# Optimization experiments

Hardware: AMD Instinct MI355X
Metric: run time of the kernel (lower is better)

The kernel has to match this reference:

```python
import jax, jax.numpy as jnp
import numpy as np

HARD_ANGLE = 15.0  # degrees, from PMLoss __init__ default
NUM_CLASSES = 22
NUM_POINTS = 2048
BATCH = 32


def quat_to_rotmat(q):
    # q: [..., 4] in (w, x, y, z) order (PoseCNN convention); assumes unit norm
    w, x, y, z = q[..., 0], q[..., 1], q[..., 2], q[..., 3]
    R = jnp.stack([
        1 - 2 * (y * y + z * z), 2 * (x * y - z * w), 2 * (x * z + y * w),
        2 * (x * y + z * w), 1 - 2 * (x * x + z * z), 2 * (y * z - x * w),
        2 * (x * z - y * w), 2 * (y * z + x * w), 1 - 2 * (x * x + y * y)],
        axis=-1)
    return R.reshape(q.shape[:-1] + (3, 3))


def smooth_l1(x):
    ax = jnp.abs(x)
    return jnp.where(ax < 1.0, 0.5 * x * x, ax - 0.5)


def setup_inputs() -> dict:
    key = jax.random.key(0)
    k1, k2, k3, k4 = jax.random.split(key, 4)
    B, C, P = BATCH, NUM_CLASSES, NUM_POINTS
    # unit quaternions per (sample, class)
    q_pred = jax.random.normal(k1, (B, C, 4), dtype=jnp.float32)
    q_pred = q_pred / jnp.linalg.norm(q_pred, axis=-1, keepdims=True)
    q_gt = jax.random.normal(k2, (B, C, 4), dtype=jnp.float32)
    q_gt = q_gt / jnp.linalg.norm(q_gt, axis=-1, keepdims=True)
    prediction = q_pred.reshape(B, 4 * C)
    target = q_gt.reshape(B, 4 * C)
    # one active class per sample: weight block of ones at that class
    cls = jax.random.randint(k3, (B,), 1, C)  # skip background class 0
    weight = jnp.zeros((B, C, 4), dtype=jnp.float32)
    weight = weight.at[jnp.arange(B), cls, :].set(1.0).reshape(B, 4 * C)
    # model point clouds, roughly object-scale (~10 cm)
    points = 0.1 * jax.random.normal(k4, (C, P, 3), dtype=jnp.float32)
    # half the classes symmetric
    symmetry = (jnp.arange(C) % 2).astype(jnp.float32)
    return {"prediction": prediction, "target": target, "weight": weight,
            "points": points, "symmetry": symmetry}


def reference(prediction, target, weight, points, symmetry):
    B = prediction.shape[0]
    C = symmetry.shape[0]
    P = points.shape[1]
    # class per sample = first class with weight > 0 (CUDA scans stride-4 w slot)
    wsel = weight.reshape(B, C, 4)[:, :, 0]           # [B, C]
    cls = jnp.argmax(wsel > 0, axis=1)                # [B]
    valid = (jnp.max(wsel, axis=1) > 0)               # [B] samples with a class
    bidx = jnp.arange(B)
    q_pred = prediction.reshape(B, C, 4)[bidx, cls]   # [B, 4]
    q_gt = target.reshape(B, C, 4)[bidx, cls]         # [B, 4]
    R_pred = quat_to_rotmat(q_pred)                   # [B, 3, 3]
    R_gt = quat_to_rotmat(q_gt)
    pts = points[cls]                                 # [B, P, 3]
    p_pred = jnp.einsum('bij,bpj->bpi', R_pred, pts)  # [B, P, 3]
    p_gt = jnp.einsum('bij,bpj->bpi', R_gt, pts)      # [B, P, 3]
    # angular distance between quaternions, in degrees
    dot = jnp.abs(jnp.sum(q_pred * q_gt, axis=1))
    ang = 2.0 * jnp.arccos(jnp.clip(dot, 0.0, 1.0)) * (180.0 / jnp.pi)
    use_closest = (symmetry[cls] > 0) & (ang > HARD_ANGLE)  # [B]
    # pairwise squared distances without materializing [B,P,P,3]
    d2 = (jnp.sum(p_pred * p_pred, axis=-1)[:, :, None]
          + jnp.sum(p_gt * p_gt, axis=-1)[:, None, :]
          - 2.0 * jnp.einsum('bpi,bqi->bpq', p_pred, p_gt))  # [B, P, P]
    nn_idx = jnp.argmin(d2, axis=-1)                         # [B, P]
    p_gt_nn = jnp.take_along_axis(p_gt, nn_idx[..., None], axis=1)
    matched = jnp.where(use_closest[:, None, None], p_gt_nn, p_gt)
    diff = p_pred - matched                                   # [B, P, 3]
    per_sample = jnp.sum(smooth_l1(diff), axis=(1, 2)) * valid.astype(diff.dtype)
    loss = jnp.sum(per_sample) / jnp.asarray(B * P, dtype=diff.dtype)
    return loss
```

## Files before the change

### kernel.cpp

```cpp
#include <hip/hip_runtime.h>

#define NPTS 2048
#define QC 32
#define G  (NPTS / QC)
#define RP 8
#define HARD_COS 0.9914448613738104f
#define META_FLOATS 24
#define PRED_OFF 1024

__global__ void pm_prep(const float* __restrict__ pred,
                        const float* __restrict__ tgt,
                        const float* __restrict__ wgt,
                        const float* __restrict__ sym,
                        float* __restrict__ ws,
                        float* __restrict__ out,
                        int B, int C) {
    int b = blockIdx.x * blockDim.x + threadIdx.x;
    if (b == 0) out[0] = 0.0f;
    if (b >= B) return;

    int cls = 0; float valid = 0.0f;
    for (int c = 0; c < C; ++c) {
        if (wgt[b * 4 * C + c * 4] > 0.0f) { cls = c; valid = 1.0f; break; }
    }
    const float* qp = pred + b * 4 * C + cls * 4;
    const float* qg = tgt  + b * 4 * C + cls * 4;
    float pw = qp[0], px = qp[1], py = qp[2], pz = qp[3];
    float gw = qg[0], gx = qg[1], gy = qg[2], gz = qg[3];

    float* o = ws + (size_t)b * META_FLOATS;
    o[0] = 1.f - 2.f * (py * py + pz * pz);
    o[1] = 2.f * (px * py - pz * pw);
    o[2] = 2.f * (px * pz + py * pw);
    o[3] = 2.f * (px * py + pz * pw);
    o[4] = 1.f - 2.f * (px * px + pz * pz);
    o[5] = 2.f * (py * pz - px * pw);
    o[6] = 2.f * (px * pz - py * pw);
    o[7] = 2.f * (py * pz + px * pw);
    o[8] = 1.f - 2.f * (px * px + py * py);
    o[9]  = 1.f - 2.f * (gy * gy + gz * gz);
    o[10] = 2.f * (gx * gy - gz * gw);
    o[11] = 2.f * (gx * gz + gy * gw);
    o[12] = 2.f * (gx * gy + gz * gw);
    o[13] = 1.f - 2.f * (gx * gx + gz * gz);
    o[14] = 2.f * (gy * gz - gx * gw);
    o[15] = 2.f * (gx * gz - gy * gw);
    o[16] = 2.f * (gy * gz + gx * gw);
    o[17] = 1.f - 2.f * (gx * gx + gy * gy);

    float dot = fabsf(pw * gw + px * gx + py * gy + pz * gz);
    dot = fminf(fmaxf(dot, 0.0f), 1.0f);
    float uc = (sym[cls] > 0.0f && dot < HARD_COS) ? 1.0f : 0.0f;
    o[18] = (float)cls;
    o[19] = valid;
    o[20] = uc;
}

__global__ __launch_bounds__(256) void pm_rotate(const float* __restrict__ points,
                                                 float* __restrict__ ws,
                                                 int gt_off) {
    const int b = blockIdx.y;
    const int side = blockIdx.x;
    const float* o = ws + (size_t)b * META_FLOATS;
    if (o[19] == 0.0f) return;
    const int mbase = (side == 0) ? 0 : 9;
    const float m0 = o[mbase + 0], m1 = o[mbase + 1], m2 = o[mbase + 2],
                m3 = o[mbase + 3], m4 = o[mbase + 4], m5 = o[mbase + 5],
                m6 = o[mbase + 6], m7 = o[mbase + 7], m8 = o[mbase + 8];
    const int cls = (int)o[18];
    const float* pts = points + (size_t)cls * NPTS * 3;
    float4* dst = (float4*)(ws + (side == 0 ? PRED_OFF : gt_off)) + (size_t)b * NPTS;
    const int tid = threadIdx.x;
#pragma unroll
    for (int r = 0; r < RP; ++r) {
        int i = r * 256 + tid;
        float x = pts[i * 3 + 0], y = pts[i * 3 + 1], z = pts[i * 3 + 2];
        float ax = m0 * x + m1 * y + m2 * z;
        float ay = m3 * x + m4 * y + m5 * z;
        float az = m6 * x + m7 * y + m8 * z;
        float w = (side == 0) ? 0.0f : (ax * ax + ay * ay + az * az);
        dst[i] = make_float4(ax, ay, az, w);
    }
}

__global__ __launch_bounds__(256) void pm_partial(float* __restrict__ ws,
                                                  int gt_off, int cand_off) {
    const int b  = blockIdx.y;
    const int qc = blockIdx.x;
    const float* o = ws + (size_t)b * META_FLOATS;
    if (o[19] == 0.0f || o[20] == 0.0f) return;

    const float4* pred_rot = (const float4*)(ws + PRED_OFF) + (size_t)b * NPTS;
    const float4* gt_rot   = (const float4*)(ws + gt_off)   + (size_t)b * NPTS;
    const int tid = threadIdx.x;

    __shared__ float4 gt[G];
    if (tid < G) gt[tid] = gt_rot[qc * G + tid];
    __syncthreads();

    float nx[RP], ny[RP], nz[RP], bd[RP];
    int bi[RP];
#pragma unroll
    for (int r = 0; r < RP; ++r) {
        float4 pp = pred_rot[r * 256 + tid];
        nx[r] = -2.0f * pp.x; ny[r] = -2.0f * pp.y; nz[r] = -2.0f * pp.z;
        bd[r] = 3.4e38f; bi[r] = 0;
    }

#pragma unroll 4
    for (int j = 0; j < G; ++j) {
        float4 g = gt[j];
#pragma unroll
        for (int r = 0; r < RP; ++r) {
            float d = __fmaf_rn(nx[r], g.x,
                      __fmaf_rn(ny[r], g.y,
                      __fmaf_rn(nz[r], g.z, g.w)));
            if (d < bd[r]) { bd[r] = d; bi[r] = j; }
        }
    }

    float* cand = ws + cand_off + ((size_t)b * QC + qc) * NPTS;
#pragma unroll
    for (int r = 0; r < RP; ++r) {
        int p = r * 256 + tid;
        cand[p] = (float)(qc * G + bi[r]);
    }
}

__device__ __forceinline__ float smooth_l1(float x) {
    float ax = fabsf(x);
    return (ax < 1.0f) ? 0.5f * x * x : ax - 0.5f;
}

__global__ __launch_bounds__(256) void pm_final(float* __restrict__ ws,
                                                float* __restrict__ out,
                                                int gt_off, int cand_off,
                                                float inv_bp) {
    __shared__ float partial[4];
    const int b = blockIdx.y;
    const float* o = ws + (size_t)b * META_FLOATS;
    const int tid = threadIdx.x;
    float acc = 0.0f;

    if (o[19] != 0.0f) {
        const float4* pred_rot = (const float4*)(ws + PRED_OFF) + (size_t)b * NPTS;
        const float4* gt_rot   = (const float4*)(ws + gt_off)   + (size_t)b * NPTS;
        const int p = blockIdx.x * 256 + tid;
        float4 pp = pred_rot[p];
        float mx, my, mz;
        if (o[20] != 0.0f) {
            const float nx = -2.0f * pp.x, ny = -2.0f * pp.y, nz = -2.0f * pp.z;
            const float* cand = ws + cand_off + (size_t)b * QC * NPTS + p;
            float bd = 3.4e38f; int bq = 0;
#pragma unroll 8
            for (int qc = 0; qc < QC; ++qc) {
                int q = (int)cand[(size_t)qc * NPTS];
                float4 g = gt_rot[q];
                float d = __fmaf_rn(nx, g.x,
                          __fmaf_rn(ny, g.y,
                          __fmaf_rn(nz, g.z, g.w)));
                if (d < bd) { bd = d; bq = q; }
            }
            float4 g = gt_rot[bq];
            mx = g.x; my = g.y; mz = g.z;
        } else {
            float4 g = gt_rot[p];
            mx = g.x; my = g.y; mz = g.z;
        }
        acc = smooth_l1(pp.x - mx) + smooth_l1(pp.y - my) + smooth_l1(pp.z - mz);
    }

    for (int off = 32; off > 0; off >>= 1) acc += __shfl_down(acc, off);
    if ((tid & 63) == 0) partial[tid >> 6] = acc;
    __syncthreads();
    if (tid == 0) {
        float s = partial[0] + partial[1] + partial[2] + partial[3];
        atomicAdd(out, s * inv_bp);
    }
}

extern "C" void kernel_launch(void* const* d_in, const int* in_sizes, int n_in,
                              void* d_out, int out_size, void* d_ws, size_t ws_size,
                              hipStream_t stream) {
    const float* pred = (const float*)d_in[0];
    const float* tgt  = (const float*)d_in[1];
    const float* wgt  = (const float*)d_in[2];
    const float* pts  = (const float*)d_in[3];
    const float* sym  = (const float*)d_in[4];
    float* out = (float*)d_out;
    float* ws  = (float*)d_ws;

    const int C = in_sizes[4];
    const int B = in_sizes[0] / (4 * C);

    const int gt_off   = PRED_OFF + B * NPTS * 4;
    const int cand_off = gt_off   + B * NPTS * 4;

    pm_prep<<<1, 64, 0, stream>>>(pred, tgt, wgt, sym, ws, out, B, C);
    dim3 gridR(2, B);
    pm_rotate<<<gridR, 256, 0, stream>>>(pts, ws, gt_off);
    dim3 gridP(QC, B);
    pm_partial<<<gridP, 256, 0, stream>>>(ws, gt_off, cand_off);
    dim3 gridF(NPTS / 256, B);
    pm_final<<<gridF, 256, 0, stream>>>(ws, out, gt_off, cand_off,
                                        1.0f / (float)(B * NPTS));
}
```

Baseline: 95.56 us.

## Collapse four kernels into two and scan nearest neighbours directly from global memory

Replaces the prep/rotate/partial/final pipeline with two kernels. The first rotates the ground-truth points, finding the class with a wave ballot. The second recomputes the predicted rotation inline and runs a full 2048-point nearest-neighbour scan per point, reading from global memory. This removes two launches and the candidate-index buffer round trip. In exchange, each symmetric sample's argmin search now runs on only 8 blocks instead of 32 chunked blocks, losing shared-memory reuse and the chunk-level parallelism.

New measurement: 223.1 us. 133% more time.

```diff
diff --git a/kernel.cpp b/kernel.cpp
--- a/kernel.cpp
+++ b/kernel.cpp
@@ -1,173 +1,119 @@
 #include <hip/hip_runtime.h>
 
 #define NPTS 2048
-#define QC 32
-#define G  (NPTS / QC)
-#define RP 8
 #define HARD_COS 0.9914448613738104f
-#define META_FLOATS 24
-#define PRED_OFF 1024
 
-__global__ void pm_prep(const float* __restrict__ pred,
-                        const float* __restrict__ tgt,
-                        const float* __restrict__ wgt,
-                        const float* __restrict__ sym,
-                        float* __restrict__ ws,
-                        float* __restrict__ out,
-                        int B, int C) {
-    int b = blockIdx.x * blockDim.x + threadIdx.x;
-    if (b == 0) out[0] = 0.0f;
-    if (b >= B) return;
-
-    int cls = 0; float valid = 0.0f;
-    for (int c = 0; c < C; ++c) {
-        if (wgt[b * 4 * C + c * 4] > 0.0f) { cls = c; valid = 1.0f; break; }
-    }
-    const float* qp = pred + b * 4 * C + cls * 4;
-    const float* qg = tgt  + b * 4 * C + cls * 4;
-    float pw = qp[0], px = qp[1], py = qp[2], pz = qp[3];
-    float gw = qg[0], gx = qg[1], gy = qg[2], gz = qg[3];
-
-    float* o = ws + (size_t)b * META_FLOATS;
-    o[0] = 1.f - 2.f * (py * py + pz * pz);
-    o[1] = 2.f * (px * py - pz * pw);
-    o[2] = 2.f * (px * pz + py * pw);
-    o[3] = 2.f * (px * py + pz * pw);
-    o[4] = 1.f - 2.f * (px * px + pz * pz);
-    o[5] = 2.f * (py * pz - px * pw);
-    o[6] = 2.f * (px * pz - py * pw);
-    o[7] = 2.f * (py * pz + px * pw);
-    o[8] = 1.f - 2.f * (px * px + py * py);
-    o[9]  = 1.f - 2.f * (gy * gy + gz * gz);
-    o[10] = 2.f * (gx * gy - gz * gw);
-    o[11] = 2.f * (gx * gz + gy * gw);
-    o[12] = 2.f * (gx * gy + gz * gw);
-    o[13] = 1.f - 2.f * (gx * gx + gz * gz);
-    o[14] = 2.f * (gy * gz - gx * gw);
-    o[15] = 2.f * (gx * gz - gy * gw);
-    o[16] = 2.f * (gy * gz + gx * gw);
-    o[17] = 1.f - 2.f * (gx * gx + gy * gy);
-
-    float dot = fabsf(pw * gw + px * gx + py * gy + pz * gz);
-    dot = fminf(fmaxf(dot, 0.0f), 1.0f);
-    float uc = (sym[cls] > 0.0f && dot < HARD_COS) ? 1.0f : 0.0f;
-    o[18] = (float)cls;
-    o[19] = valid;
-    o[20] = uc;
-}
-
-__global__ __launch_bounds__(256) void pm_rotate(const float* __restrict__ points,
-                                                 float* __restrict__ ws,
-                                                 int gt_off) {
-    const int b = blockIdx.y;
-    const int side = blockIdx.x;
-    const float* o = ws + (size_t)b * META_FLOATS;
-    if (o[19] == 0.0f) return;
-    const int mbase = (side == 0) ? 0 : 9;
-    const float m0 = o[mbase + 0], m1 = o[mbase + 1], m2 = o[mbase + 2],
-                m3 = o[mbase + 3], m4 = o[mbase + 4], m5 = o[mbase + 5],
-                m6 = o[mbase + 6], m7 = o[mbase + 7], m8 = o[mbase + 8];
-    const int cls = (int)o[18];
-    const float* pts = points + (size_t)cls * NPTS * 3;
-    float4* dst = (float4*)(ws + (side == 0 ? PRED_OFF : gt_off)) + (size_t)b * NPTS;
-    const int tid = threadIdx.x;
-#pragma unroll
-    for (int r = 0; r < RP; ++r) {
-        int i = r * 256 + tid;
-        float x = pts[i * 3 + 0], y = pts[i * 3 + 1], z = pts[i * 3 + 2];
-        float ax = m0 * x + m1 * y + m2 * z;
-        float ay = m3 * x + m4 * y + m5 * z;
-        float az = m6 * x + m7 * y + m8 * z;
-        float w = (side == 0) ? 0.0f : (ax * ax + ay * ay + az * az);
-        dst[i] = make_float4(ax, ay, az, w);
-    }
-}
-
-__global__ __launch_bounds__(256) void pm_partial(float* __restrict__ ws,
-                                                  int gt_off, int cand_off) {
-    const int b  = blockIdx.y;
-    const int qc = blockIdx.x;
-    const float* o = ws + (size_t)b * META_FLOATS;
-    if (o[19] == 0.0f || o[20] == 0.0f) return;
-
-    const float4* pred_rot = (const float4*)(ws + PRED_OFF) + (size_t)b * NPTS;
-    const float4* gt_rot   = (const float4*)(ws + gt_off)   + (size_t)b * NPTS;
-    const int tid = threadIdx.x;
-
-    __shared__ float4 gt[G];
-    if (tid < G) gt[tid] = gt_rot[qc * G + tid];
-    __syncthreads();
-
-    float nx[RP], ny[RP], nz[RP], bd[RP];
-    int bi[RP];
-#pragma unroll
-    for (int r = 0; r < RP; ++r) {
-        float4 pp = pred_rot[r * 256 + tid];
-        nx[r] = -2.0f * pp.x; ny[r] = -2.0f * pp.y; nz[r] = -2.0f * pp.z;
-        bd[r] = 3.4e38f; bi[r] = 0;
-    }
-
-#pragma unroll 4
-    for (int j = 0; j < G; ++j) {
-        float4 g = gt[j];
-#pragma unroll
-        for (int r = 0; r < RP; ++r) {
-            float d = __fmaf_rn(nx[r], g.x,
-                      __fmaf_rn(ny[r], g.y,
-                      __fmaf_rn(nz[r], g.z, g.w)));
-            if (d < bd[r]) { bd[r] = d; bi[r] = j; }
-        }
-    }
-
-    float* cand = ws + cand_off + ((size_t)b * QC + qc) * NPTS;
-#pragma unroll
-    for (int r = 0; r < RP; ++r) {
-        int p = r * 256 + tid;
-        cand[p] = (float)(qc * G + bi[r]);
-    }
-}
 
 __device__ __forceinline__ float smooth_l1(float x) {
     float ax = fabsf(x);
     return (ax < 1.0f) ? 0.5f * x * x : ax - 0.5f;
 }
 
-__global__ __launch_bounds__(256) void pm_final(float* __restrict__ ws,
+__global__ __launch_bounds__(256) void pm_rotgt(const float* __restrict__ tgt,
+                                                const float* __restrict__ wgt,
+                                                const float* __restrict__ pts,
+                                                float* __restrict__ ws,
                                                 float* __restrict__ out,
-                                                int gt_off, int cand_off,
-                                                float inv_bp) {
+                                                int C) {
+    const int b = blockIdx.y;
+    const int tid = threadIdx.x;
+    if (blockIdx.x == 0 && b == 0 && tid == 0) out[0] = 0.0f;
+
+    const int lane = tid & 63;
+    bool has = (lane < C) && (wgt[(size_t)b * 4 * C + (size_t)lane * 4] > 0.0f);
+    unsigned long long m = __ballot(has);
+    if (m == 0ull) return;
+    const int cls = (int)__ffsll((unsigned long long)m) - 1;
+
+    const float* qg = tgt + (size_t)b * 4 * C + (size_t)cls * 4;
+    const float gw = qg[0], gx = qg[1], gy = qg[2], gz = qg[3];
+    const float m0 = 1.f - 2.f * (gy * gy + gz * gz);
+    const float m1 = 2.f * (gx * gy - gz * gw);
+    const float m2 = 2.f * (gx * gz + gy * gw);
+    const float m3 = 2.f * (gx * gy + gz * gw);
+    const float m4 = 1.f - 2.f * (gx * gx + gz * gz);
+    const float m5 = 2.f * (gy * gz - gx * gw);
+    const float m6 = 2.f * (gx * gz - gy * gw);
+    const float m7 = 2.f * (gy * gz + gx * gw);
+    const float m8 = 1.f - 2.f * (gx * gx + gy * gy);
+
+    const float* p = pts + (size_t)cls * NPTS * 3;
+    float4* dst = (float4*)ws + (size_t)b * NPTS;
+    const int i = blockIdx.x * 256 + tid;
+    const float x = p[i * 3 + 0], y = p[i * 3 + 1], z = p[i * 3 + 2];
+    const float ax = m0 * x + m1 * y + m2 * z;
+    const float ay = m3 * x + m4 * y + m5 * z;
+    const float az = m6 * x + m7 * y + m8 * z;
+    const float w = ax * ax + ay * ay + az * az;
+    dst[i] = make_float4(ax, ay, az, w);
+}
+
+__global__ __launch_bounds__(256) void pm_loss(const float* __restrict__ pred,
+                                               const float* __restrict__ tgt,
+                                               const float* __restrict__ wgt,
+                                               const float* __restrict__ pts,
+                                               const float* __restrict__ sym,
+                                               const float* __restrict__ ws,
+                                               float* __restrict__ out,
+                                               int C, float inv_bp) {
     __shared__ float partial[4];
     const int b = blockIdx.y;
-    const float* o = ws + (size_t)b * META_FLOATS;
     const int tid = threadIdx.x;
+    const int lane = tid & 63;
+
+    bool has = (lane < C) && (wgt[(size_t)b * 4 * C + (size_t)lane * 4] > 0.0f);
+    unsigned long long mm = __ballot(has);
     float acc = 0.0f;
 
-    if (o[19] != 0.0f) {
-        const float4* pred_rot = (const float4*)(ws + PRED_OFF) + (size_t)b * NPTS;
-        const float4* gt_rot   = (const float4*)(ws + gt_off)   + (size_t)b * NPTS;
+    if (mm != 0ull) {
+        const int cls = (int)__ffsll((unsigned long long)mm) - 1;
+        const float* qp = pred + (size_t)b * 4 * C + (size_t)cls * 4;
+        const float* qg = tgt  + (size_t)b * 4 * C + (size_t)cls * 4;
+        const float pw = qp[0], px = qp[1], py = qp[2], pz = qp[3];
+        const float gw = qg[0], gx = qg[1], gy = qg[2], gz = qg[3];
+
+        const float r0 = 1.f - 2.f * (py * py + pz * pz);
+        const float r1 = 2.f * (px * py - pz * pw);
+        const float r2 = 2.f * (px * pz + py * pw);
+        const float r3 = 2.f * (px * py + pz * pw);
+        const float r4 = 1.f - 2.f * (px * px + pz * pz);
+        const float r5 = 2.f * (py * pz - px * pw);
+        const float r6 = 2.f * (px * pz - py * pw);
+        const float r7 = 2.f * (py * pz + px * pw);
+        const float r8 = 1.f - 2.f * (px * px + py * py);
+
+        float dot = fabsf(pw * gw + px * gx + py * gy + pz * gz);
+        dot = fminf(fmaxf(dot, 0.0f), 1.0f);
+        const bool uc = (sym[cls] > 0.0f) && (dot < HARD_COS);
+
         const int p = blockIdx.x * 256 + tid;
-        float4 pp = pred_rot[p];
+        const float* pp = pts + (size_t)cls * NPTS * 3 + (size_t)p * 3;
+        const float x = pp[0], y = pp[1], z = pp[2];
+        const float ppx = r0 * x + r1 * y + r2 * z;
+        const float ppy = r3 * x + r4 * y + r5 * z;
+        const float ppz = r6 * x + r7 * y + r8 * z;
+
+        const float4* gtb = (const float4*)ws + (size_t)b * NPTS;
         float mx, my, mz;
-        if (o[20] != 0.0f) {
-            const float nx = -2.0f * pp.x, ny = -2.0f * pp.y, nz = -2.0f * pp.z;
-            const float* cand = ws + cand_off + (size_t)b * QC * NPTS + p;
-            float bd = 3.4e38f; int bq = 0;
+        if (uc) {
+            const float nx = -2.0f * ppx, ny = -2.0f * ppy, nz = -2.0f * ppz;
+            float bd = 3.4e38f;
+            int bj = 0;
 #pragma unroll 8
-            for (int qc = 0; qc < QC; ++qc) {
-                int q = (int)cand[(size_t)qc * NPTS];
-                float4 g = gt_rot[q];
+            for (int j = 0; j < NPTS; ++j) {
+                float4 g = gtb[j];
                 float d = __fmaf_rn(nx, g.x,
                           __fmaf_rn(ny, g.y,
                           __fmaf_rn(nz, g.z, g.w)));
-                if (d < bd) { bd = d; bq = q; }
+                if (d < bd) { bd = d; bj = j; }
             }
-            float4 g = gt_rot[bq];
+            float4 g = gtb[bj];
             mx = g.x; my = g.y; mz = g.z;
         } else {
-            float4 g = gt_rot[p];
+            float4 g = gtb[p];
             mx = g.x; my = g.y; mz = g.z;
         }
-        acc = smooth_l1(pp.x - mx) + smooth_l1(pp.y - my) + smooth_l1(pp.z - mz);
+        acc = smooth_l1(ppx - mx) + smooth_l1(ppy - my) + smooth_l1(ppz - mz);
     }
 
     for (int off = 32; off > 0; off >>= 1) acc += __shfl_down(acc, off);
@@ -193,15 +139,8 @@
     const int C = in_sizes[4];
     const int B = in_sizes[0] / (4 * C);
 
-    const int gt_off   = PRED_OFF + B * NPTS * 4;
-    const int cand_off = gt_off   + B * NPTS * 4;
-
-    pm_prep<<<1, 64, 0, stream>>>(pred, tgt, wgt, sym, ws, out, B, C);
-    dim3 gridR(2, B);
-    pm_rotate<<<gridR, 256, 0, stream>>>(pts, ws, gt_off);
-    dim3 gridP(QC, B);
-    pm_partial<<<gridP, 256, 0, stream>>>(ws, gt_off, cand_off);
-    dim3 gridF(NPTS / 256, B);
-    pm_final<<<gridF, 256, 0, stream>>>(ws, out, gt_off, cand_off,
-                                        1.0f / (float)(B * NPTS));
+    dim3 grid(NPTS / 256, B);
+    pm_rotgt<<<grid, 256, 0, stream>>>(tgt, wgt, pts, ws, out, C);
+    pm_loss<<<grid, 256, 0, stream>>>(pred, tgt, wgt, pts, sym, ws, out, C,
+                                      1.0f / (float)(B * NPTS));
 }
```
